# Optimization experiments

Measured on AMD Instinct MI355X. Metric: run time of the kernel, lower is better.

The kernel has to match this reference:

```python
import jax, jax.numpy as jnp
import numpy as np

# Pauli-Z expectation table: sign of bit w in 4-bit index (wire 0 = MSB, axis order q0..q3)
_idx = np.arange(16)
_bits = (_idx[None, :] >> (3 - np.arange(4))[:, None]) & 1
_Z_TABLE = (1.0 - 2.0 * _bits).astype(np.float32)  # (4, 16)


def _apply_ry(state, theta, wire):
    # state: (N, 2,2,2,2) real amplitudes; RY = [[c,-s],[s,c]], c=cos(t/2), s=sin(t/2)
    ax = 1 + wire
    c = jnp.cos(theta / 2)
    s = jnp.sin(theta / 2)
    st = jnp.moveaxis(state, ax, 1)
    s0, s1 = st[:, 0], st[:, 1]
    st = jnp.stack([c * s0 - s * s1, s * s0 + c * s1], axis=1)
    return jnp.moveaxis(st, 1, ax)


def _apply_cnot(state, control, target):
    # flips the target axis on the control==1 slice (assumes target > control)
    ac, at = 1 + control, 1 + target
    s0 = jnp.take(state, 0, axis=ac)
    s1 = jnp.flip(jnp.take(state, 1, axis=ac), axis=at - 1)
    return jnp.stack([s0, s1], axis=ac)


def setup_inputs() -> dict:
    key = jax.random.key(0)
    ks = jax.random.split(key, 8)
    B = 8192
    x = jax.random.uniform(ks[0], (B, 1, 28, 28), dtype=jnp.float32)
    conv_w = jax.random.normal(ks[1], (4, 1, 2, 2), dtype=jnp.float32) * 0.5
    conv_b = jax.random.normal(ks[2], (4,), dtype=jnp.float32) * 0.1
    bn_gamma = jnp.ones((4,), jnp.float32)
    bn_beta = jnp.zeros((4,), jnp.float32)
    bn_mean = jnp.zeros((4,), jnp.float32)
    bn_var = jnp.ones((4,), jnp.float32)
    shortcut_weight = jnp.float32(1.0)
    theta = jax.random.normal(ks[3], (8,), dtype=jnp.float32)  # 8 trainable RY angles
    lin_w = jax.random.normal(ks[4], (10, 784), dtype=jnp.float32) * 0.03
    lin_b = jnp.zeros((10,), jnp.float32)
    log_scale = jnp.float32(1.0)
    return {"x": x, "conv_w": conv_w, "conv_b": conv_b, "bn_gamma": bn_gamma,
            "bn_beta": bn_beta, "bn_mean": bn_mean, "bn_var": bn_var,
            "shortcut_weight": shortcut_weight, "theta": theta,
            "lin_w": lin_w, "lin_b": lin_b, "log_scale": log_scale}


def reference(x, conv_w, conv_b, bn_gamma, bn_beta, bn_mean, bn_var,
              shortcut_weight, theta, lin_w, lin_b, log_scale):
    B = x.shape[0]
    # classical shortcut: conv(1->4, k2, s2) + BN (eval mode, running stats)
    sc = jax.lax.conv_general_dilated(
        x, conv_w, window_strides=(2, 2), padding='VALID',
        dimension_numbers=('NCHW', 'OIHW', 'NCHW')) + conv_b[None, :, None, None]
    sc = (sc - bn_mean[None, :, None, None]) * jax.lax.rsqrt(bn_var[None, :, None, None] + 1e-5)
    sc = sc * bn_gamma[None, :, None, None] + bn_beta[None, :, None, None]
    sc = sc.reshape(B, -1)  # (B, 784) channel-major, matches torch .view

    # extract 2x2 patches in (r, c) scan order -> (B*196, 4) with order [tl, tr, bl, br]
    img = x.reshape(B, 28, 28)
    patches = img.reshape(B, 14, 2, 14, 2).transpose(0, 1, 3, 2, 4).reshape(B * 196, 4)

    # RY encoding of |0000>: product state, amplitudes [cos(v/2), sin(v/2)] per wire
    half = patches * 0.5
    e = jnp.stack([jnp.cos(half), jnp.sin(half)], axis=-1)  # (N, 4, 2)
    state = jnp.einsum('na,nb,nc,nd->nabcd', e[:, 0], e[:, 1], e[:, 2], e[:, 3])

    # parameterized circuit: RY layer, CNOT(0,1), CNOT(2,3), RY layer
    for w in range(4):
        state = _apply_ry(state, theta[w], w)
    state = _apply_cnot(state, 0, 1)
    state = _apply_cnot(state, 2, 3)
    for w in range(4):
        state = _apply_ry(state, theta[4 + w], w)

    # <Z_w> expectations (real amplitudes -> probs = state**2)
    probs = (state ** 2).reshape(-1, 16)        # (B*196, 16)
    meas = probs @ jnp.asarray(_Z_TABLE).T      # (B*196, 4)
    qfeat = meas.reshape(B, 196 * 4)            # cat order: patch-major, wires inner

    feat = shortcut_weight * sc + qfeat
    logits = (feat @ lin_w.T + lin_b) * log_scale  # dropout is identity in eval
    return jax.nn.log_softmax(logits, axis=-1)
```

## Files before the change

### kernel.cpp

```cpp
#include <hip/hip_runtime.h>
#include <hip/hip_fp16.h>
#include <math.h>

#define BLOCK 256
#define WAVES 4
#define IPW   2
#define LWS   792
#define FEATS 792

typedef _Float16 h2v __attribute__((ext_vector_type(2)));

__device__ __forceinline__ float dot2h(unsigned a, unsigned b, float c) {
#if __has_builtin(__builtin_amdgcn_fdot2)
    return __builtin_amdgcn_fdot2(__builtin_bit_cast(h2v, a),
                                  __builtin_bit_cast(h2v, b), c, false);
#else
    h2v xa = __builtin_bit_cast(h2v, a), yb = __builtin_bit_cast(h2v, b);
    return c + (float)xa[0] * (float)yb[0] + (float)xa[1] * (float)yb[1];
#endif
}

__device__ __forceinline__ unsigned packh(float a, float b) {
    __half2 h = __float22half2_rn(make_float2(a, b));
    return __builtin_bit_cast(unsigned, h);
}

__global__ __launch_bounds__(BLOCK) void quanv_fused2(
    const float* __restrict__ x,
    const float* __restrict__ conv_w,
    const float* __restrict__ conv_b,
    const float* __restrict__ bn_gamma,
    const float* __restrict__ bn_beta,
    const float* __restrict__ bn_mean,
    const float* __restrict__ bn_var,
    const float* __restrict__ sw_p,
    const float* __restrict__ theta,
    const float* __restrict__ lin_w,
    const float* __restrict__ lin_b,
    const float* __restrict__ log_scale_p,
    float* __restrict__ out)
{
    __shared__ __half lw[10 * LWS];
    __shared__ __half feat[WAVES][FEATS];

    const int t = threadIdx.x;
    const int lane = t & 63, wv = t >> 6;
    __half* fw = &feat[wv][0];

    for (int g = t * 4; g < 7840; g += BLOCK * 4) {
        float4 v = *(const float4*)(lin_w + g);
        int k = g / 784, f = g - k * 784;
        uint2 pk;
        pk.x = packh(v.x, v.y);
        pk.y = packh(v.z, v.w);
        *(uint2*)&lw[k * LWS + f] = pk;
    }

    const float sw = sw_p[0];
    const float ls = log_scale_p[0];
    float wf[4][4], bf[4];
#pragma unroll
    for (int c = 0; c < 4; ++c) {
        float scale = bn_gamma[c] * rsqrtf(bn_var[c] + 1e-5f);
        float sws = sw * scale;
#pragma unroll
        for (int k = 0; k < 4; ++k) wf[c][k] = sws * conv_w[c * 4 + k];
        bf[c] = sw * (scale * (conv_b[c] - bn_mean[c]) + bn_beta[c]);
    }
    const float th0 = theta[0], th1 = theta[1], th2 = theta[2], th3 = theta[3];
    float s4, c4, s5, c5, s6, c6, s7, c7;
    __sincosf(0.5f * theta[4], &s4, &c4);
    __sincosf(0.5f * theta[5], &s5, &c5);
    __sincosf(0.5f * theta[6], &s6, &c6);
    __sincosf(0.5f * theta[7], &s7, &c7);

    auto pair_meas = [&](float xa, float xb, float tha, float thb,
                         float sE, float cE, float sF, float cF,
                         float& mA, float& mB) {
        float sA, cA, sB, cB;
        __sincosf(0.5f * (xa + tha), &sA, &cA);
        __sincosf(0.5f * (xb + thb), &sB, &cB);
        float cc = cA * cB, ss = sA * sB, cs = cA * sB, sc_ = sA * cB;
        float u0 = cE * cc - sE * ss;
        float u1 = cE * cs - sE * sc_;
        float u2 = sE * cc + cE * ss;
        float u3 = sE * cs + cE * sc_;
        float v0 = cF * u0 - sF * u1, v1 = sF * u0 + cF * u1;
        float v2 = cF * u2 - sF * u3, v3 = sF * u2 + cF * u3;
        mA = u0 * u0 + u1 * u1 - u2 * u2 - u3 * u3;
        mB = v0 * v0 - v1 * v1 + v2 * v2 - v3 * v3;
    };

    float2 px[8];
    auto load_pix = [&](int img) {
        const float* xb = x + (size_t)img * 784;
#pragma unroll
        for (int j = 0; j < 4; ++j) {
            int p = lane + 64 * j; if (p > 195) p = 195;
            int i = p / 14, jj = p - i * 14;
            px[2 * j]     = *(const float2*)(xb + (2 * i) * 28 + 2 * jj);
            px[2 * j + 1] = *(const float2*)(xb + (2 * i + 1) * 28 + 2 * jj);
        }
    };

    const int img0 = (blockIdx.x * WAVES + wv) * IPW;
    load_pix(img0);

    for (int it = 0; it < IPW; ++it) {
        const int img = img0 + it;
        unsigned q0[4], q1[4];

#pragma unroll
        for (int j = 0; j < 3; ++j) {
            const int p = lane + 64 * j;
            float x00 = px[2 * j].x, x01 = px[2 * j].y;
            float x10 = px[2 * j + 1].x, x11 = px[2 * j + 1].y;
            float m0, m1, m2, m3;
            pair_meas(x00, x01, th0, th1, s4, c4, s5, c5, m0, m1);
            pair_meas(x10, x11, th2, th3, s6, c6, s7, c7, m2, m3);
            q0[j] = packh(m0, m1);
            q1[j] = packh(m2, m3);
#pragma unroll
            for (int c = 0; c < 4; ++c)
                fw[c * 196 + p] = __float2half(
                    wf[c][0] * x00 + wf[c][1] * x01 +
                    wf[c][2] * x10 + wf[c][3] * x11 + bf[c]);
        }
        if (lane < 4) {
            const int p = lane + 192;
            float x00 = px[6].x, x01 = px[6].y;
            float x10 = px[7].x, x11 = px[7].y;
            float m0, m1, m2, m3;
            pair_meas(x00, x01, th0, th1, s4, c4, s5, c5, m0, m1);
            pair_meas(x10, x11, th2, th3, s6, c6, s7, c7, m2, m3);
            q0[3] = packh(m0, m1);
            q1[3] = packh(m2, m3);
#pragma unroll
            for (int c = 0; c < 4; ++c)
                fw[c * 196 + p] = __float2half(
                    wf[c][0] * x00 + wf[c][1] * x01 +
                    wf[c][2] * x10 + wf[c][3] * x11 + bf[c]);
        }

        if (it + 1 < IPW) load_pix(img + 1);

        __syncthreads();

#pragma unroll
        for (int j = 0; j < 3; ++j) {
            const int p = lane + 64 * j;
            uint2 v = *(uint2*)&fw[4 * p];
            __half2 a0 = __builtin_bit_cast(__half2, v.x);
            __half2 a1 = __builtin_bit_cast(__half2, v.y);
            a0 = __hadd2(a0, __builtin_bit_cast(__half2, q0[j]));
            a1 = __hadd2(a1, __builtin_bit_cast(__half2, q1[j]));
            v.x = __builtin_bit_cast(unsigned, a0);
            v.y = __builtin_bit_cast(unsigned, a1);
            *(uint2*)&fw[4 * p] = v;
        }
        if (lane < 4) {
            const int p = lane + 192;
            uint2 v = *(uint2*)&fw[4 * p];
            __half2 a0 = __builtin_bit_cast(__half2, v.x);
            __half2 a1 = __builtin_bit_cast(__half2, v.y);
            a0 = __hadd2(a0, __builtin_bit_cast(__half2, q0[3]));
            a1 = __hadd2(a1, __builtin_bit_cast(__half2, q1[3]));
            v.x = __builtin_bit_cast(unsigned, a0);
            v.y = __builtin_bit_cast(unsigned, a1);
            *(uint2*)&fw[4 * p] = v;
        }

        __syncthreads();

        float acc = 0.f;
        if (lane < 60) {
            const int k = lane / 6, c = lane - k * 6;
            const int start = c * 136;
            const int nit = (c == 5) ? 13 : 17;
            const uint4* fp = (const uint4*)&fw[start];
            const uint4* wp = (const uint4*)&lw[k * LWS + start];
            for (int i = 0; i < nit; ++i) {
                uint4 a = fp[i], b = wp[i];
                acc = dot2h(a.x, b.x, acc);
                acc = dot2h(a.y, b.y, acc);
                acc = dot2h(a.z, b.z, acc);
                acc = dot2h(a.w, b.w, acc);
            }
        }
        float s1 = acc + __shfl_down(acc, 1);
        float s2 = s1 + __shfl_down(s1, 2);
        float tot = s2 + __shfl_down(s1, 4);

        float logit = 0.f;
        if (lane < 60 && lane % 6 == 0)
            logit = (tot + lin_b[lane / 6]) * ls;

        float m = -1e30f;
        float lg;
#pragma unroll
        for (int kk = 0; kk < 10; ++kk) {
            float v = __shfl(logit, kk * 6);
            m = fmaxf(m, v);
        }
        float ssum = 0.f;
#pragma unroll
        for (int kk = 0; kk < 10; ++kk) {
            float v = __shfl(logit, kk * 6);
            ssum += __expf(v - m);
        }
        const float lse = m + __logf(ssum);
        lg = __shfl(logit, 6 * lane);
        if (lane < 10) out[(size_t)img * 10 + lane] = lg - lse;

        __syncthreads();
    }
}

extern "C" void kernel_launch(void* const* d_in, const int* in_sizes, int n_in,
                              void* d_out, int out_size, void* d_ws, size_t ws_size,
                              hipStream_t stream) {
    const float* x         = (const float*)d_in[0];
    const float* conv_w    = (const float*)d_in[1];
    const float* conv_b    = (const float*)d_in[2];
    const float* bn_gamma  = (const float*)d_in[3];
    const float* bn_beta   = (const float*)d_in[4];
    const float* bn_mean   = (const float*)d_in[5];
    const float* bn_var    = (const float*)d_in[6];
    const float* sw        = (const float*)d_in[7];
    const float* theta     = (const float*)d_in[8];
    const float* lin_w     = (const float*)d_in[9];
    const float* lin_b     = (const float*)d_in[10];
    const float* log_scale = (const float*)d_in[11];
    float* out = (float*)d_out;

    const int B = in_sizes[0] / 784;
    dim3 grid(B / (WAVES * IPW)), block(BLOCK);
    hipLaunchKernelGGL(quanv_fused2, grid, block, 0, stream,
                       x, conv_w, conv_b, bn_gamma, bn_beta, bn_mean, bn_var,
                       sw, theta, lin_w, lin_b, log_scale, out);
}
```

Baseline: 19.99 us.

## Simplify quantum measurement algebra and restructure linear layer as per-lane dot with DPP reductions

The per-patch circuit expectation is replaced by a closed-form expression that needs fewer multiplies and uses full-angle sincos. Both images per wave are now processed together in one pass, which removes the loop, the extra barriers and the LDS read-modify-write of features. The linear layer is reorganised so each lane accumulates all 10 logits over its own patches and then reduces across the wave with DPP. Softmax is computed redundantly in every lane, and occupancy is raised with a launch-bounds hint. In exchange there are more registers per lane and 20 wave reductions per wave.

```diff
diff --git a/kernel.cpp b/kernel.cpp
--- a/kernel.cpp
+++ b/kernel.cpp
@@ -3,10 +3,7 @@
 #include <math.h>
 
 #define BLOCK 256
-#define WAVES 4
-#define IPW   2
-#define LWS   792
-#define FEATS 792
+#define WVS   4
 
 typedef _Float16 h2v __attribute__((ext_vector_type(2)));
 
@@ -25,7 +22,41 @@
     return __builtin_bit_cast(unsigned, h);
 }
 
-__global__ __launch_bounds__(BLOCK) void quanv_fused2(
+__device__ __forceinline__ unsigned pkadd(unsigned a, unsigned b) {
+    __half2 r = __hadd2(__builtin_bit_cast(__half2, a), __builtin_bit_cast(__half2, b));
+    return __builtin_bit_cast(unsigned, r);
+}
+
+template <int CTRL, int RMASK>
+__device__ __forceinline__ float dppadd(float x) {
+    int t = __builtin_amdgcn_update_dpp(0, __builtin_bit_cast(int, x),
+                                        CTRL, RMASK, 0xf, false);
+    return x + __builtin_bit_cast(float, t);
+}
+__device__ __forceinline__ float wave_sum64(float x) {
+    x = dppadd<0x111, 0xf>(x);
+    x = dppadd<0x112, 0xf>(x);
+    x = dppadd<0x114, 0xf>(x);
+    x = dppadd<0x118, 0xf>(x);
+    x = dppadd<0x142, 0xa>(x);
+    x = dppadd<0x143, 0xc>(x);
+    return __builtin_bit_cast(float,
+        __builtin_amdgcn_readlane(__builtin_bit_cast(int, x), 63));
+}
+
+__device__ __forceinline__ float sel10(const float L[10], int j) {
+    float a0 = (j & 1) ? L[1] : L[0];
+    float a2 = (j & 1) ? L[3] : L[2];
+    float a4 = (j & 1) ? L[5] : L[4];
+    float a6 = (j & 1) ? L[7] : L[6];
+    float a8 = (j & 1) ? L[9] : L[8];
+    float b0 = (j & 2) ? a2 : a0;
+    float b4 = (j & 2) ? a6 : a4;
+    float c0 = (j & 4) ? b4 : b0;
+    return (j & 8) ? a8 : c0;
+}
+
+__global__ __launch_bounds__(BLOCK, 4) void quanv_fused4(
     const float* __restrict__ x,
     const float* __restrict__ conv_w,
     const float* __restrict__ conv_b,
@@ -40,24 +71,42 @@
     const float* __restrict__ log_scale_p,
     float* __restrict__ out)
 {
-    __shared__ __half lw[10 * LWS];
-    __shared__ __half feat[WAVES][FEATS];
+    __shared__ __half lw[10 * 784];
+    __shared__ __half fsc[WVS][2][784];
 
     const int t = threadIdx.x;
     const int lane = t & 63, wv = t >> 6;
-    __half* fw = &feat[wv][0];
-
-    for (int g = t * 4; g < 7840; g += BLOCK * 4) {
-        float4 v = *(const float4*)(lin_w + g);
-        int k = g / 784, f = g - k * 784;
+    const int img0 = (blockIdx.x * WVS + wv) * 2;
+
+    int off[4];
+#pragma unroll
+    for (int j = 0; j < 4; ++j) {
+        int p = (j < 3) ? (lane + 64 * j) : (192 + (lane & 3));
+        int i = p / 14, jj = p - i * 14;
+        off[j] = i * 56 + jj * 2;
+    }
+    const float* xb0 = x + (size_t)img0 * 784;
+    const float* xb1 = xb0 + 784;
+    float2 pxa[4][2], pxb[4][2];
+#pragma unroll
+    for (int j = 0; j < 4; ++j) {
+        pxa[j][0] = *(const float2*)(xb0 + off[j]);
+        pxa[j][1] = *(const float2*)(xb0 + off[j] + 28);
+        pxb[j][0] = *(const float2*)(xb1 + off[j]);
+        pxb[j][1] = *(const float2*)(xb1 + off[j] + 28);
+    }
+
+    for (int q = t; q < 1960; q += BLOCK) {
+        float4 v = *(const float4*)(lin_w + q * 4);
+        int k = q / 196;
+        int f = q * 4 - k * 784;
         uint2 pk;
         pk.x = packh(v.x, v.y);
         pk.y = packh(v.z, v.w);
-        *(uint2*)&lw[k * LWS + f] = pk;
-    }
-
-    const float sw = sw_p[0];
-    const float ls = log_scale_p[0];
+        *(uint2*)&lw[k * 784 + f] = pk;
+    }
+
+    const float sw = sw_p[0], ls = log_scale_p[0];
     float wf[4][4], bf[4];
 #pragma unroll
     for (int c = 0; c < 4; ++c) {
@@ -68,152 +117,114 @@
         bf[c] = sw * (scale * (conv_b[c] - bn_mean[c]) + bn_beta[c]);
     }
     const float th0 = theta[0], th1 = theta[1], th2 = theta[2], th3 = theta[3];
-    float s4, c4, s5, c5, s6, c6, s7, c7;
-    __sincosf(0.5f * theta[4], &s4, &c4);
-    __sincosf(0.5f * theta[5], &s5, &c5);
-    __sincosf(0.5f * theta[6], &s6, &c6);
-    __sincosf(0.5f * theta[7], &s7, &c7);
-
-    auto pair_meas = [&](float xa, float xb, float tha, float thb,
-                         float sE, float cE, float sF, float cF,
-                         float& mA, float& mB) {
-        float sA, cA, sB, cB;
-        __sincosf(0.5f * (xa + tha), &sA, &cA);
-        __sincosf(0.5f * (xb + thb), &sB, &cB);
-        float cc = cA * cB, ss = sA * sB, cs = cA * sB, sc_ = sA * cB;
-        float u0 = cE * cc - sE * ss;
-        float u1 = cE * cs - sE * sc_;
-        float u2 = sE * cc + cE * ss;
-        float u3 = sE * cs + cE * sc_;
-        float v0 = cF * u0 - sF * u1, v1 = sF * u0 + cF * u1;
-        float v2 = cF * u2 - sF * u3, v3 = sF * u2 + cF * u3;
-        mA = u0 * u0 + u1 * u1 - u2 * u2 - u3 * u3;
-        mB = v0 * v0 - v1 * v1 + v2 * v2 - v3 * v3;
+    float sE0, cE0, sF0, cF0, sE1, cE1, sF1, cF1;
+    __sincosf(theta[4], &sE0, &cE0);
+    __sincosf(theta[5], &sF0, &cF0);
+    __sincosf(theta[6], &sE1, &cE1);
+    __sincosf(theta[7], &sF1, &cF1);
+
+    auto qmeas = [&](float xa, float xbv, float tha, float thb,
+                     float sE, float cE, float sF, float cF,
+                     float& mA, float& mB) {
+        float sa, ca, sb, cb;
+        __sincosf(xa + tha, &sa, &ca);
+        __sincosf(xbv + thb, &sb, &cb);
+        mA = cE * ca - sE * (sa * sb);
+        mB = cF * (ca * cb) - sF * sb;
     };
 
-    float2 px[8];
-    auto load_pix = [&](int img) {
-        const float* xb = x + (size_t)img * 784;
-#pragma unroll
-        for (int j = 0; j < 4; ++j) {
-            int p = lane + 64 * j; if (p > 195) p = 195;
-            int i = p / 14, jj = p - i * 14;
-            px[2 * j]     = *(const float2*)(xb + (2 * i) * 28 + 2 * jj);
-            px[2 * j + 1] = *(const float2*)(xb + (2 * i + 1) * 28 + 2 * jj);
-        }
-    };
-
-    const int img0 = (blockIdx.x * WAVES + wv) * IPW;
-    load_pix(img0);
-
-    for (int it = 0; it < IPW; ++it) {
-        const int img = img0 + it;
-        unsigned q0[4], q1[4];
-
-#pragma unroll
-        for (int j = 0; j < 3; ++j) {
-            const int p = lane + 64 * j;
-            float x00 = px[2 * j].x, x01 = px[2 * j].y;
-            float x10 = px[2 * j + 1].x, x11 = px[2 * j + 1].y;
+    unsigned qa[4][2], qb[4][2];
+#pragma unroll
+    for (int j = 0; j < 4; ++j) {
+        if (j == 3 && lane >= 4) break;
+        const int p = (j < 3) ? (lane + 64 * j) : (192 + lane);
+        {
+            float x00 = pxa[j][0].x, x01 = pxa[j][0].y;
+            float x10 = pxa[j][1].x, x11 = pxa[j][1].y;
             float m0, m1, m2, m3;
-            pair_meas(x00, x01, th0, th1, s4, c4, s5, c5, m0, m1);
-            pair_meas(x10, x11, th2, th3, s6, c6, s7, c7, m2, m3);
-            q0[j] = packh(m0, m1);
-            q1[j] = packh(m2, m3);
+            qmeas(x00, x01, th0, th1, sE0, cE0, sF0, cF0, m0, m1);
+            qmeas(x10, x11, th2, th3, sE1, cE1, sF1, cF1, m2, m3);
+            qa[j][0] = packh(m0, m1);
+            qa[j][1] = packh(m2, m3);
 #pragma unroll
             for (int c = 0; c < 4; ++c)
-                fw[c * 196 + p] = __float2half(
+                fsc[wv][0][c * 196 + p] = __float2half(
                     wf[c][0] * x00 + wf[c][1] * x01 +
                     wf[c][2] * x10 + wf[c][3] * x11 + bf[c]);
         }
-        if (lane < 4) {
-            const int p = lane + 192;
-            float x00 = px[6].x, x01 = px[6].y;
-            float x10 = px[7].x, x11 = px[7].y;
+        {
+            float x00 = pxb[j][0].x, x01 = pxb[j][0].y;
+            float x10 = pxb[j][1].x, x11 = pxb[j][1].y;
             float m0, m1, m2, m3;
-            pair_meas(x00, x01, th0, th1, s4, c4, s5, c5, m0, m1);
-            pair_meas(x10, x11, th2, th3, s6, c6, s7, c7, m2, m3);
-            q0[3] = packh(m0, m1);
-            q1[3] = packh(m2, m3);
+            qmeas(x00, x01, th0, th1, sE0, cE0, sF0, cF0, m0, m1);
+            qmeas(x10, x11, th2, th3, sE1, cE1, sF1, cF1, m2, m3);
+            qb[j][0] = packh(m0, m1);
+            qb[j][1] = packh(m2, m3);
 #pragma unroll
             for (int c = 0; c < 4; ++c)
-                fw[c * 196 + p] = __float2half(
+                fsc[wv][1][c * 196 + p] = __float2half(
                     wf[c][0] * x00 + wf[c][1] * x01 +
                     wf[c][2] * x10 + wf[c][3] * x11 + bf[c]);
         }
-
-        if (it + 1 < IPW) load_pix(img + 1);
-
-        __syncthreads();
-
-#pragma unroll
-        for (int j = 0; j < 3; ++j) {
-            const int p = lane + 64 * j;
-            uint2 v = *(uint2*)&fw[4 * p];
-            __half2 a0 = __builtin_bit_cast(__half2, v.x);
-            __half2 a1 = __builtin_bit_cast(__half2, v.y);
-            a0 = __hadd2(a0, __builtin_bit_cast(__half2, q0[j]));
-            a1 = __hadd2(a1, __builtin_bit_cast(__half2, q1[j]));
-            v.x = __builtin_bit_cast(unsigned, a0);
-            v.y = __builtin_bit_cast(unsigned, a1);
-            *(uint2*)&fw[4 * p] = v;
+    }
+
+    __syncthreads();
+
+    float acc0[10], acc1[10];
+#pragma unroll
+    for (int k = 0; k < 10; ++k) { acc0[k] = 0.f; acc1[k] = 0.f; }
+
+#pragma unroll
+    for (int j = 0; j < 4; ++j) {
+        if (j == 3 && lane >= 4) break;
+        const int p = (j < 3) ? (lane + 64 * j) : (192 + lane);
+        uint2 f0 = *(uint2*)&fsc[wv][0][4 * p];
+        uint2 f1 = *(uint2*)&fsc[wv][1][4 * p];
+        const unsigned fa0 = pkadd(f0.x, qa[j][0]);
+        const unsigned fa1 = pkadd(f0.y, qa[j][1]);
+        const unsigned fb0 = pkadd(f1.x, qb[j][0]);
+        const unsigned fb1 = pkadd(f1.y, qb[j][1]);
+        const __half* wrow = &lw[4 * p];
+#pragma unroll
+        for (int k = 0; k < 10; ++k) {
+            uint2 w = *(const uint2*)&wrow[k * 784];
+            acc0[k] = dot2h(fa0, w.x, acc0[k]);
+            acc0[k] = dot2h(fa1, w.y, acc0[k]);
+            acc1[k] = dot2h(fb0, w.x, acc1[k]);
+            acc1[k] = dot2h(fb1, w.y, acc1[k]);
         }
-        if (lane < 4) {
-            const int p = lane + 192;
-            uint2 v = *(uint2*)&fw[4 * p];
-            __half2 a0 = __builtin_bit_cast(__half2, v.x);
-            __half2 a1 = __builtin_bit_cast(__half2, v.y);
-            a0 = __hadd2(a0, __builtin_bit_cast(__half2, q0[3]));
-            a1 = __hadd2(a1, __builtin_bit_cast(__half2, q1[3]));
-            v.x = __builtin_bit_cast(unsigned, a0);
-            v.y = __builtin_bit_cast(unsigned, a1);
-            *(uint2*)&fw[4 * p] = v;
-        }
-
-        __syncthreads();
-
-        float acc = 0.f;
-        if (lane < 60) {
-            const int k = lane / 6, c = lane - k * 6;
-            const int start = c * 136;
-            const int nit = (c == 5) ? 13 : 17;
-            const uint4* fp = (const uint4*)&fw[start];
-            const uint4* wp = (const uint4*)&lw[k * LWS + start];
-            for (int i = 0; i < nit; ++i) {
-                uint4 a = fp[i], b = wp[i];
-                acc = dot2h(a.x, b.x, acc);
-                acc = dot2h(a.y, b.y, acc);
-                acc = dot2h(a.z, b.z, acc);
-                acc = dot2h(a.w, b.w, acc);
-            }
-        }
-        float s1 = acc + __shfl_down(acc, 1);
-        float s2 = s1 + __shfl_down(s1, 2);
-        float tot = s2 + __shfl_down(s1, 4);
-
-        float logit = 0.f;
-        if (lane < 60 && lane % 6 == 0)
-            logit = (tot + lin_b[lane / 6]) * ls;
-
-        float m = -1e30f;
-        float lg;
-#pragma unroll
-        for (int kk = 0; kk < 10; ++kk) {
-            float v = __shfl(logit, kk * 6);
-            m = fmaxf(m, v);
-        }
-        float ssum = 0.f;
-#pragma unroll
-        for (int kk = 0; kk < 10; ++kk) {
-            float v = __shfl(logit, kk * 6);
-            ssum += __expf(v - m);
-        }
-        const float lse = m + __logf(ssum);
-        lg = __shfl(logit, 6 * lane);
-        if (lane < 10) out[(size_t)img * 10 + lane] = lg - lse;
-
-        __syncthreads();
-    }
+    }
+
+    float L0[10], L1[10];
+#pragma unroll
+    for (int k = 0; k < 10; ++k) {
+        L0[k] = wave_sum64(acc0[k]);
+        L1[k] = wave_sum64(acc1[k]);
+    }
+#pragma unroll
+    for (int k = 0; k < 10; ++k) {
+        const float bk = lin_b[k];
+        L0[k] = (L0[k] + bk) * ls;
+        L1[k] = (L1[k] + bk) * ls;
+    }
+
+    float mA = L0[0], mB = L1[0];
+#pragma unroll
+    for (int k = 1; k < 10; ++k) { mA = fmaxf(mA, L0[k]); mB = fmaxf(mB, L1[k]); }
+    float eA = 0.f, eB = 0.f;
+#pragma unroll
+    for (int k = 0; k < 10; ++k) {
+        eA += __expf(L0[k] - mA);
+        eB += __expf(L1[k] - mB);
+    }
+    const float lseA = mA + __logf(eA);
+    const float lseB = mB + __logf(eB);
+
+    const int j = lane & 15;
+    if (lane < 10)
+        out[(size_t)img0 * 10 + j] = sel10(L0, j) - lseA;
+    else if (lane >= 16 && lane < 26)
+        out[(size_t)(img0 + 1) * 10 + j] = sel10(L1, j) - lseB;
 }
 
 extern "C" void kernel_launch(void* const* d_in, const int* in_sizes, int n_in,
@@ -234,8 +245,8 @@
     float* out = (float*)d_out;
 
     const int B = in_sizes[0] / 784;
-    dim3 grid(B / (WAVES * IPW)), block(BLOCK);
-    hipLaunchKernelGGL(quanv_fused2, grid, block, 0, stream,
+    dim3 grid(B / (WVS * 2)), block(BLOCK);
+    hipLaunchKernelGGL(quanv_fused4, grid, block, 0, stream,
                        x, conv_w, conv_b, bn_gamma, bn_beta, bn_mean, bn_var,
                        sw, theta, lin_w, lin_b, log_scale, out);
 }
```

New measurement: 21.74 us. +8.7%, slower.
